# Kernel optimization log

Measured on AMD Instinct MI355X. Metric: run time of the kernel, lower is better.

The kernel has to match this reference:

```python
import jax, jax.numpy as jnp
import numpy as np

B, T, H, D = 1, 2048, 32, 128
Q_GROUP = 4
HKV = H // Q_GROUP
INNER = H * D
KV_INNER = HKV * D
ROPE_BASE = 10000.0
NEG = -1e30


def _rope_tables(seq_len, head_dim, dtype):
    inv_freq = 1.0 / (ROPE_BASE ** (jnp.arange(0, head_dim, 2, dtype=jnp.float32) / head_dim))
    t = jnp.arange(seq_len, dtype=jnp.float32)
    freqs = jnp.einsum('t,f->tf', t, inv_freq)          # [T, D/2]
    emb = jnp.concatenate([freqs, freqs], axis=-1)      # [T, D]
    cos = jnp.cos(emb)[None, :, None, :].astype(dtype)  # [1, T, 1, D]
    sin = jnp.sin(emb)[None, :, None, :].astype(dtype)
    return cos, sin


def _rotate(x, cos, sin):
    # x: [B, T, H, D]; split-half rotation: cat(-x2, x1)
    half = x.shape[-1] // 2
    x1, x2 = x[..., :half], x[..., half:]
    x_rot = jnp.concatenate([-x2, x1], axis=-1)
    return x * cos + x_rot * sin


def setup_inputs() -> dict:
    key = jax.random.key(0)
    ks = jax.random.split(key, 5)
    return {
        'stm': jax.random.normal(ks[0], (B, T, H, D), dtype=jnp.float32),
        'w_q': jax.random.normal(ks[1], (INNER, INNER), dtype=jnp.float32) * 0.02,
        'w_k': jax.random.normal(ks[2], (KV_INNER, INNER), dtype=jnp.float32) * 0.02,
        'w_v': jax.random.normal(ks[3], (KV_INNER, INNER), dtype=jnp.float32) * 0.02,
        'w_o': jax.random.normal(ks[4], (INNER, INNER), dtype=jnp.float32) * 0.02,
    }


def reference(stm, w_q, w_k, w_v, w_o):
    b, t, h, d = stm.shape
    x = stm.reshape(b * t, h * d)
    q = x @ w_q.T                                   # [B*T, H*D]
    k = x @ w_k.T                                   # [B*T, Hkv*D]
    v = x @ w_v.T
    # GQA repeat_interleave over query-group axis (broadcast then reshape)
    k = jnp.broadcast_to(k.reshape(b * t, HKV, 1, d), (b * t, HKV, Q_GROUP, d)).reshape(b, t, h, d)
    v = jnp.broadcast_to(v.reshape(b * t, HKV, 1, d), (b * t, HKV, Q_GROUP, d)).reshape(b, t, h, d)
    q = q.reshape(b, t, h, d)
    cos, sin = _rope_tables(t, d, stm.dtype)        # prefill: seq_start = 0
    q = _rotate(q, cos, sin)
    k = _rotate(k, cos, sin)                        # rotated k is what gets written to the KV cache
    scale = 1.0 / np.sqrt(d)
    scores = jnp.einsum('bqhd,bkhd->bhqk', q, k).astype(jnp.float32) * scale
    causal = jnp.tril(jnp.ones((t, t), dtype=jnp.float32))          # mask_w
    bias = (1.0 - causal) * NEG                                     # mask_b
    scores = scores * causal[None, None] + bias[None, None]
    attn = jax.nn.softmax(scores, axis=-1).astype(stm.dtype)
    o = jnp.einsum('bhqk,bkhd->bqhd', attn, v)
    o = o.reshape(b * t, h * d) @ w_o.T
    return o.reshape(b, t, h, d)
```

## Files before the change

kernel.cpp:

```cpp
#include <hip/hip_runtime.h>
#include <hip/hip_bf16.h>
#include <stdint.h>
#include <stddef.h>

using bf16  = __hip_bfloat16;
using v4s   = __attribute__((ext_vector_type(4))) short;
using v8s   = __attribute__((ext_vector_type(8))) short;
using f32x4 = __attribute__((ext_vector_type(4))) float;

#define MFMA_16x16x32(a, b, c) __builtin_amdgcn_mfma_f32_16x16x32_bf16((a), (b), (c), 0, 0, 0)

__device__ __forceinline__ void async_lds16(const bf16* g, bf16* l) {
  __builtin_amdgcn_global_load_lds(
      (const __attribute__((address_space(1))) void*)g,
      (__attribute__((address_space(3))) void*)l, 16, 0, 0);
}

__device__ __forceinline__ short bf16_bits(float f) {
  bf16 h = __float2bfloat16(f);
  short s;
  __builtin_memcpy(&s, &h, sizeof(s));
  return s;
}

__global__ void cvt_f32_bf16(const float* __restrict__ in, bf16* __restrict__ out,
                             int n4) {
  const int i = blockIdx.x * blockDim.x + threadIdx.x;
  if (i >= n4) return;
  const float4 f = ((const float4*)in)[i];
  v4s o;
  o[0] = bf16_bits(f.x);
  o[1] = bf16_bits(f.y);
  o[2] = bf16_bits(f.z);
  o[3] = bf16_bits(f.w);
  *(v4s*)(out + (size_t)i * 4) = o;
}

template <bool F32OUT>
__global__ __launch_bounds__(512, 2) void gemm_bt8(const bf16* __restrict__ A,
                                                   const bf16* __restrict__ B,
                                                   void* __restrict__ C,
                                                   int M, int N, int K) {
  __shared__ bf16 lds[2][64][512];
  const int tid  = threadIdx.x;
  const int w    = tid >> 6;
  const int lane = tid & 63;
  const int quad = lane >> 4;
  const int m16  = lane & 15;
  const int wr = w >> 2, wc = w & 3;
  const int tm = blockIdx.y, tn = blockIdx.x;
  const int NKT = K >> 6;

  const bf16* Ast0 = A + (size_t)(tm * 256 + w * 16 + m16) * K + quad * 8;
  const bf16* Ast1 = Ast0 + (size_t)128 * K;
  const bf16* Bst0 = B + (size_t)(tn * 256 + w * 16 + m16) * K + quad * 8;
  const bf16* Bst1 = Bst0 + (size_t)128 * K;

  auto stage = [&](const bf16* g, bf16* l) {
    async_lds16(g, l);
    async_lds16(g + 32, l + 512);
  };

  f32x4 acc[8][4] = {};

  {
    bf16* L0 = &lds[0][0][0];
    bf16* L1 = &lds[1][0][0];
    stage(Bst0, L0 + (32 + w * 2) * 512);
    stage(Bst1, L0 + (48 + w * 2) * 512);
    stage(Ast0, L0 + (w * 2) * 512);
    stage(Ast1, L0 + (16 + w * 2) * 512);
    stage(Bst0 + 64, L1 + (32 + w * 2) * 512);
    stage(Bst1 + 64, L1 + (48 + w * 2) * 512);
    stage(Ast0 + 64, L1 + (w * 2) * 512);
  }
  asm volatile("s_waitcnt vmcnt(6)" ::: "memory");
  __builtin_amdgcn_s_barrier();

  for (int k = 0; k < NKT; ++k) {
    bf16* Lc = &lds[k & 1][0][0];
    bf16* Ln = &lds[(k & 1) ^ 1][0][0];
    v8s af[4][2], bfv[4][2];
#pragma unroll
    for (int mi = 0; mi < 4; ++mi) {
      af[mi][0] = *(const v8s*)(Lc + ((wr * 8 + mi) * 2 + 0) * 512 + lane * 8);
      af[mi][1] = *(const v8s*)(Lc + ((wr * 8 + mi) * 2 + 1) * 512 + lane * 8);
    }
#pragma unroll
    for (int ni = 0; ni < 4; ++ni) {
      bfv[ni][0] = *(const v8s*)(Lc + (32 + (wc * 4 + ni) * 2 + 0) * 512 + lane * 8);
      bfv[ni][1] = *(const v8s*)(Lc + (32 + (wc * 4 + ni) * 2 + 1) * 512 + lane * 8);
    }
    if (k + 1 < NKT) stage(Ast1 + (size_t)(k + 1) * 64, Ln + (16 + w * 2) * 512);
    __builtin_amdgcn_s_barrier();
    asm volatile("s_waitcnt lgkmcnt(0)" ::: "memory");
    __builtin_amdgcn_sched_barrier(0);
    __builtin_amdgcn_s_setprio(1);
#pragma unroll
    for (int mi = 0; mi < 4; ++mi)
#pragma unroll
      for (int ni = 0; ni < 2; ++ni) {
        acc[mi][ni] = MFMA_16x16x32(af[mi][0], bfv[ni][0], acc[mi][ni]);
        acc[mi][ni] = MFMA_16x16x32(af[mi][1], bfv[ni][1], acc[mi][ni]);
      }
    __builtin_amdgcn_s_setprio(0);
    __builtin_amdgcn_s_barrier();
    if (k + 2 < NKT) stage(Bst0 + (size_t)(k + 2) * 64, Lc + (32 + w * 2) * 512);
    __builtin_amdgcn_s_barrier();
    __builtin_amdgcn_s_setprio(1);
#pragma unroll
    for (int mi = 0; mi < 4; ++mi)
#pragma unroll
      for (int ni = 2; ni < 4; ++ni) {
        acc[mi][ni] = MFMA_16x16x32(af[mi][0], bfv[ni][0], acc[mi][ni]);
        acc[mi][ni] = MFMA_16x16x32(af[mi][1], bfv[ni][1], acc[mi][ni]);
      }
    __builtin_amdgcn_s_setprio(0);
    __builtin_amdgcn_s_barrier();
#pragma unroll
    for (int mi = 0; mi < 4; ++mi) {
      af[mi][0] = *(const v8s*)(Lc + ((wr * 8 + 4 + mi) * 2 + 0) * 512 + lane * 8);
      af[mi][1] = *(const v8s*)(Lc + ((wr * 8 + 4 + mi) * 2 + 1) * 512 + lane * 8);
    }
    if (k + 2 < NKT) stage(Bst1 + (size_t)(k + 2) * 64, Lc + (48 + w * 2) * 512);
    __builtin_amdgcn_s_barrier();
    asm volatile("s_waitcnt lgkmcnt(0)" ::: "memory");
    __builtin_amdgcn_sched_barrier(0);
    __builtin_amdgcn_s_setprio(1);
#pragma unroll
    for (int mi = 0; mi < 4; ++mi)
#pragma unroll
      for (int ni = 0; ni < 2; ++ni) {
        acc[4 + mi][ni] = MFMA_16x16x32(af[mi][0], bfv[ni][0], acc[4 + mi][ni]);
        acc[4 + mi][ni] = MFMA_16x16x32(af[mi][1], bfv[ni][1], acc[4 + mi][ni]);
      }
    __builtin_amdgcn_s_setprio(0);
    __builtin_amdgcn_s_barrier();
    if (k + 2 < NKT) stage(Ast0 + (size_t)(k + 2) * 64, Lc + (w * 2) * 512);
    if (k < NKT - 2) {
      asm volatile("s_waitcnt vmcnt(6)" ::: "memory");
    } else {
      asm volatile("s_waitcnt vmcnt(0)" ::: "memory");
    }
    __builtin_amdgcn_s_barrier();
    __builtin_amdgcn_s_setprio(1);
#pragma unroll
    for (int mi = 0; mi < 4; ++mi)
#pragma unroll
      for (int ni = 2; ni < 4; ++ni) {
        acc[4 + mi][ni] = MFMA_16x16x32(af[mi][0], bfv[ni][0], acc[4 + mi][ni]);
        acc[4 + mi][ni] = MFMA_16x16x32(af[mi][1], bfv[ni][1], acc[4 + mi][ni]);
      }
    __builtin_amdgcn_s_setprio(0);
    __builtin_amdgcn_s_barrier();
  }

#pragma unroll
  for (int mi = 0; mi < 8; ++mi)
#pragma unroll
    for (int ni = 0; ni < 4; ++ni) {
      const int row = tm * 256 + wr * 128 + mi * 16 + quad * 4;
      const int col = tn * 256 + wc * 64 + ni * 16 + m16;
#pragma unroll
      for (int r = 0; r < 4; ++r) {
        if (F32OUT)
          ((float*)C)[(size_t)(row + r) * N + col] = acc[mi][ni][r];
        else
          ((bf16*)C)[(size_t)(row + r) * N + col] = __float2bfloat16(acc[mi][ni][r]);
      }
    }
}

__global__ void rope_kernel(bf16* __restrict__ qkv) {
  const int t  = blockIdx.x;
  const int hh = blockIdx.y;
  const int d  = threadIdx.x;
  const float invf = powf(10000.0f, -(float)(d & 63) * (1.0f / 64.0f));
  const float ang  = (float)t * invf;
  const float c = cosf(ang);
  const float s = sinf(ang);
  const bool isq = (hh < 32);
  bf16* ptr = qkv + (size_t)t * 6144 + (isq ? hh * 128 : 4096 + (hh - 32) * 128);
  const float x   = __bfloat162float(ptr[d]);
  const float xp  = __bfloat162float(ptr[d ^ 64]);
  __syncthreads();
  const float rot = (d < 64) ? -xp : xp;
  const float outv = (x * c + rot * s) * (isq ? 0.08838834764831845f : 1.0f);
  ptr[d] = __float2bfloat16(outv);
}

__global__ void vtrans_kernel(const bf16* __restrict__ qkv, bf16* __restrict__ vt) {
  __shared__ bf16 tile[32][34];
  const int t0 = blockIdx.x * 32, c0 = blockIdx.y * 32;
  const int tx = threadIdx.x, ty = threadIdx.y;
#pragma unroll
  for (int i = 0; i < 4; ++i)
    tile[ty + 8 * i][tx] = qkv[(size_t)(t0 + ty + 8 * i) * 6144 + 5120 + c0 + tx];
  __syncthreads();
#pragma unroll
  for (int i = 0; i < 4; ++i)
    vt[(size_t)(c0 + ty + 8 * i) * 2048 + t0 + tx] = tile[tx][ty + 8 * i];
}

__global__ __launch_bounds__(256) void attn_fused4(const bf16* __restrict__ QKV,
                                                   const bf16* __restrict__ Vt,
                                                   bf16* __restrict__ O) {
  const int bx = (int)blockIdx.x;
  const int h  = (int)blockIdx.y;
  const int qt = (h < 16) ? (15 - bx) : bx;
  const int hk = h >> 2;
  const int tid = threadIdx.x, w = tid >> 6, lane = tid & 63;
  const int quad = lane >> 4, m16 = lane & 15;
  __shared__ bf16 Ks[32 * 512];
  __shared__ bf16 Vs[32 * 512];
  __shared__ __attribute__((aligned(16))) short Ps[4][2048];
  short* Pw = Ps[w];

  v8s qf[2][4];
#pragma unroll
  for (int ni = 0; ni < 2; ++ni)
#pragma unroll
    for (int dk = 0; dk < 4; ++dk)
      qf[ni][dk] = *(const v8s*)(QKV + (size_t)(qt * 128 + w * 32 + ni * 16 + m16) * 6144 +
                                 h * 128 + dk * 32 + quad * 8);

  const bf16* kg = QKV + (size_t)m16 * 6144 + 4096 + hk * 128 + w * 32 + quad * 8;
  const bf16* vg = Vt + (size_t)(hk * 128 + m16) * 2048 + w * 32 + quad * 8;

  f32x4 acc[8][2] = {};
  float m_run[2] = {-1e30f, -1e30f}, l_run[2] = {0.f, 0.f};

#pragma unroll
  for (int mi = 0; mi < 8; ++mi)
    async_lds16(kg + (size_t)mi * 16 * 6144, &Ks[(mi * 4 + w) * 512]);
#pragma unroll
  for (int mi = 0; mi < 8; ++mi)
    async_lds16(vg + (size_t)mi * 16 * 2048, &Vs[(mi * 4 + w) * 512]);

  for (int kt = 0; kt <= qt; ++kt) {
    asm volatile("s_waitcnt vmcnt(8)" ::: "memory");
    __builtin_amdgcn_s_barrier();
    f32x4 s[8][2];
    __builtin_amdgcn_s_setprio(1);
#pragma unroll
    for (int mi = 0; mi < 8; ++mi) {
      s[mi][0] = f32x4{0.f, 0.f, 0.f, 0.f};
      s[mi][1] = f32x4{0.f, 0.f, 0.f, 0.f};
#pragma unroll
      for (int dk = 0; dk < 4; ++dk) {
        v8s af = *(const v8s*)&Ks[(mi * 4 + dk) * 512 + lane * 8];
        s[mi][0] = MFMA_16x16x32(af, qf[0][dk], s[mi][0]);
        s[mi][1] = MFMA_16x16x32(af, qf[1][dk], s[mi][1]);
      }
    }
    __builtin_amdgcn_s_setprio(0);
    asm volatile("s_waitcnt vmcnt(0)" ::: "memory");
    __builtin_amdgcn_s_barrier();
    if (kt < qt) {
      const bf16* kg2 = kg + (size_t)(kt + 1) * 128 * 6144;
#pragma unroll
      for (int mi = 0; mi < 8; ++mi)
        async_lds16(kg2 + (size_t)mi * 16 * 6144, &Ks[(mi * 4 + w) * 512]);
    }
    if (kt == qt) {
#pragma unroll
      for (int mi = 0; mi < 8; ++mi)
#pragma unroll
        for (int ni = 0; ni < 2; ++ni)
#pragma unroll
          for (int r = 0; r < 4; ++r)
            if (mi * 16 + quad * 4 + r > w * 32 + ni * 16 + m16) s[mi][ni][r] = -1e30f;
    }
#pragma unroll
    for (int ni = 0; ni < 2; ++ni) {
      float mx = -1e30f;
#pragma unroll
      for (int mi = 0; mi < 8; ++mi)
#pragma unroll
        for (int r = 0; r < 4; ++r) mx = fmaxf(mx, s[mi][ni][r]);
      mx = fmaxf(mx, __shfl_xor(mx, 16));
      mx = fmaxf(mx, __shfl_xor(mx, 32));
      const float mnew = fmaxf(m_run[ni], mx);
      const float alpha = __expf(m_run[ni] - mnew);
      m_run[ni] = mnew;
      float rs = 0.f;
#pragma unroll
      for (int mi = 0; mi < 8; ++mi)
#pragma unroll
        for (int r = 0; r < 4; ++r) {
          const float p = __expf(s[mi][ni][r] - mnew);
          s[mi][ni][r] = p;
          rs += p;
        }
      rs += __shfl_xor(rs, 16);
      rs += __shfl_xor(rs, 32);
      l_run[ni] = l_run[ni] * alpha + rs;
#pragma unroll
      for (int mi2 = 0; mi2 < 8; ++mi2)
#pragma unroll
        for (int r = 0; r < 4; ++r) acc[mi2][ni][r] *= alpha;
    }
#pragma unroll
    for (int mi = 0; mi < 4; ++mi)
#pragma unroll
      for (int ni = 0; ni < 2; ++ni) {
        v4s p4;
#pragma unroll
        for (int r = 0; r < 4; ++r) p4[r] = bf16_bits(s[mi][ni][r]);
        const int base = (ni * 2 + (mi >> 1)) * 512 +
                         ((mi & 1) * 2 + (quad >> 1)) * 128 + m16 * 8 + (quad & 1) * 4;
        *(v4s*)&Pw[base] = p4;
      }
    asm volatile("" ::: "memory");
    __builtin_amdgcn_s_setprio(1);
#pragma unroll
    for (int kpl = 0; kpl < 2; ++kpl) {
      v8s pf0 = *(const v8s*)&Pw[(0 * 2 + kpl) * 512 + lane * 8];
      v8s pf1 = *(const v8s*)&Pw[(1 * 2 + kpl) * 512 + lane * 8];
#pragma unroll
      for (int mi2 = 0; mi2 < 8; ++mi2) {
        v8s vf = *(const v8s*)&Vs[(mi2 * 4 + kpl) * 512 + lane * 8];
        acc[mi2][0] = MFMA_16x16x32(vf, pf0, acc[mi2][0]);
        acc[mi2][1] = MFMA_16x16x32(vf, pf1, acc[mi2][1]);
      }
    }
    __builtin_amdgcn_s_setprio(0);
    asm volatile("" ::: "memory");
#pragma unroll
    for (int mi = 4; mi < 8; ++mi)
#pragma unroll
      for (int ni = 0; ni < 2; ++ni) {
        const int mloc = mi - 4;
        v4s p4;
#pragma unroll
        for (int r = 0; r < 4; ++r) p4[r] = bf16_bits(s[mi][ni][r]);
        const int base = (ni * 2 + (mloc >> 1)) * 512 +
                         ((mloc & 1) * 2 + (quad >> 1)) * 128 + m16 * 8 + (quad & 1) * 4;
        *(v4s*)&Pw[base] = p4;
      }
    asm volatile("" ::: "memory");
    __builtin_amdgcn_s_setprio(1);
#pragma unroll
    for (int kpl = 0; kpl < 2; ++kpl) {
      v8s pf0 = *(const v8s*)&Pw[(0 * 2 + kpl) * 512 + lane * 8];
      v8s pf1 = *(const v8s*)&Pw[(1 * 2 + kpl) * 512 + lane * 8];
#pragma unroll
      for (int mi2 = 0; mi2 < 8; ++mi2) {
        v8s vf = *(const v8s*)&Vs[(mi2 * 4 + 2 + kpl) * 512 + lane * 8];
        acc[mi2][0] = MFMA_16x16x32(vf, pf0, acc[mi2][0]);
        acc[mi2][1] = MFMA_16x16x32(vf, pf1, acc[mi2][1]);
      }
    }
    __builtin_amdgcn_s_setprio(0);
    asm volatile("" ::: "memory");
    __builtin_amdgcn_s_barrier();
    if (kt < qt) {
      const bf16* vg2 = vg + (size_t)(kt + 1) * 128;
#pragma unroll
      for (int mi = 0; mi < 8; ++mi)
        async_lds16(vg2 + (size_t)mi * 16 * 2048, &Vs[(mi * 4 + w) * 512]);
    }
  }
#pragma unroll
  for (int ni = 0; ni < 2; ++ni) {
    const float rl = 1.0f / l_run[ni];
    const size_t qrow = qt * 128 + w * 32 + ni * 16 + m16;
#pragma unroll
    for (int mi2 = 0; mi2 < 8; ++mi2) {
      v4s o4;
#pragma unroll
      for (int r = 0; r < 4; ++r) o4[r] = bf16_bits(acc[mi2][ni][r] * rl);
      *(v4s*)(O + qrow * 4096 + h * 128 + mi2 * 16 + quad * 4) = o4;
    }
  }
}

extern "C" void kernel_launch(void* const* d_in, const int* in_sizes, int n_in,
                              void* d_out, int out_size, void* d_ws, size_t ws_size,
                              hipStream_t stream) {
  const float* stm = (const float*)d_in[0];
  const float* w_q = (const float*)d_in[1];
  const float* w_k = (const float*)d_in[2];
  const float* w_v = (const float*)d_in[3];
  const float* w_o = (const float*)d_in[4];
  float* out = (float*)d_out;

  const size_t M_STM = (size_t)2048 * 4096;
  const size_t M_WQ  = (size_t)4096 * 4096;
  const size_t M_WK  = (size_t)1024 * 4096;

  bf16* ws      = (bf16*)d_ws;
  bf16* wqkv_bf = ws;
  bf16* wo_bf   = ws;
  bf16* vT      = ws + M_WQ;
  bf16* stm_bf  = ws + 24 * 1024 * 1024;
  bf16* o_buf   = stm_bf;
  bf16* qkv_buf = ws + 32 * 1024 * 1024;

  cvt_f32_bf16<<<(int)(M_STM / 1024), 256, 0, stream>>>(stm, stm_bf, (int)(M_STM / 4));
  cvt_f32_bf16<<<(int)(M_WQ / 1024), 256, 0, stream>>>(w_q, wqkv_bf, (int)(M_WQ / 4));
  cvt_f32_bf16<<<(int)(M_WK / 1024), 256, 0, stream>>>(w_k, wqkv_bf + M_WQ, (int)(M_WK / 4));
  cvt_f32_bf16<<<(int)(M_WK / 1024), 256, 0, stream>>>(w_v, wqkv_bf + M_WQ + M_WK, (int)(M_WK / 4));

  gemm_bt8<false><<<dim3(24, 8), 512, 0, stream>>>(stm_bf, wqkv_bf, qkv_buf, 2048, 6144, 4096);

  cvt_f32_bf16<<<(int)(M_WQ / 1024), 256, 0, stream>>>(w_o, wo_bf, (int)(M_WQ / 4));

  rope_kernel<<<dim3(2048, 40), 128, 0, stream>>>(qkv_buf);
  vtrans_kernel<<<dim3(64, 32), dim3(32, 8), 0, stream>>>(qkv_buf, vT);
  attn_fused4<<<dim3(16, 32), 256, 0, stream>>>(qkv_buf, vT, o_buf);

  gemm_bt8<true><<<dim3(16, 8), 512, 0, stream>>>(o_buf, wo_bf, out, 2048, 4096, 4096);
}
```

Baseline: 627.8 us.

## Prefetch GEMM LDS fragments across phases and precompute RoPE cos/sin table

Restructures the 8-wave GEMM main loop so A/B fragment reads from LDS for the next k-tile are issued during the current tile's MFMA phases. The B fragments are split into two register sets and the MFMA phase order is reshuffled, which removes one barrier per phase and retunes the vmcnt waits. Separately, RoPE cos/sin values are computed once per (t, freq) into a table instead of with powf/sinf/cosf in every head's thread. This costs more registers in the GEMM and carries some risk of LDS read/write hazards across the reordered barriers.

```diff
diff --git a/kernel.cpp b/kernel.cpp
--- a/kernel.cpp
+++ b/kernel.cpp
@@ -37,7 +37,7 @@
 }
 
 template <bool F32OUT>
-__global__ __launch_bounds__(512, 2) void gemm_bt8(const bf16* __restrict__ A,
+__global__ __launch_bounds__(512, 2) void gemm_bt9(const bf16* __restrict__ A,
                                                    const bf16* __restrict__ B,
                                                    void* __restrict__ C,
                                                    int M, int N, int K) {
@@ -62,6 +62,9 @@
   };
 
   f32x4 acc[8][4] = {};
+  v8s af[4][2];
+  v8s bf01[2][2];
+  v8s bf23[2][2];
 
   {
     bf16* L0 = &lds[0][0][0];
@@ -76,23 +79,28 @@
   }
   asm volatile("s_waitcnt vmcnt(6)" ::: "memory");
   __builtin_amdgcn_s_barrier();
+  {
+    bf16* L0 = &lds[0][0][0];
+#pragma unroll
+    for (int mi = 0; mi < 4; ++mi)
+#pragma unroll
+      for (int kg = 0; kg < 2; ++kg)
+        af[mi][kg] = *(const v8s*)(L0 + ((wr * 8 + mi) * 2 + kg) * 512 + lane * 8);
+#pragma unroll
+    for (int ni = 0; ni < 2; ++ni)
+#pragma unroll
+      for (int kg = 0; kg < 2; ++kg) {
+        bf01[ni][kg] = *(const v8s*)(L0 + (32 + (wc * 4 + ni) * 2 + kg) * 512 + lane * 8);
+        bf23[ni][kg] = *(const v8s*)(L0 + (32 + (wc * 4 + 2 + ni) * 2 + kg) * 512 + lane * 8);
+      }
+  }
+  asm volatile("" ::: "memory");
 
   for (int k = 0; k < NKT; ++k) {
     bf16* Lc = &lds[k & 1][0][0];
     bf16* Ln = &lds[(k & 1) ^ 1][0][0];
-    v8s af[4][2], bfv[4][2];
-#pragma unroll
-    for (int mi = 0; mi < 4; ++mi) {
-      af[mi][0] = *(const v8s*)(Lc + ((wr * 8 + mi) * 2 + 0) * 512 + lane * 8);
-      af[mi][1] = *(const v8s*)(Lc + ((wr * 8 + mi) * 2 + 1) * 512 + lane * 8);
-    }
-#pragma unroll
-    for (int ni = 0; ni < 4; ++ni) {
-      bfv[ni][0] = *(const v8s*)(Lc + (32 + (wc * 4 + ni) * 2 + 0) * 512 + lane * 8);
-      bfv[ni][1] = *(const v8s*)(Lc + (32 + (wc * 4 + ni) * 2 + 1) * 512 + lane * 8);
-    }
+    __builtin_amdgcn_s_barrier();
     if (k + 1 < NKT) stage(Ast1 + (size_t)(k + 1) * 64, Ln + (16 + w * 2) * 512);
-    __builtin_amdgcn_s_barrier();
     asm volatile("s_waitcnt lgkmcnt(0)" ::: "memory");
     __builtin_amdgcn_sched_barrier(0);
     __builtin_amdgcn_s_setprio(1);
@@ -100,30 +108,36 @@
     for (int mi = 0; mi < 4; ++mi)
 #pragma unroll
       for (int ni = 0; ni < 2; ++ni) {
-        acc[mi][ni] = MFMA_16x16x32(af[mi][0], bfv[ni][0], acc[mi][ni]);
-        acc[mi][ni] = MFMA_16x16x32(af[mi][1], bfv[ni][1], acc[mi][ni]);
-      }
-    __builtin_amdgcn_s_setprio(0);
+        acc[mi][ni] = MFMA_16x16x32(af[mi][0], bf01[ni][0], acc[mi][ni]);
+        acc[mi][ni] = MFMA_16x16x32(af[mi][1], bf01[ni][1], acc[mi][ni]);
+      }
+    __builtin_amdgcn_s_setprio(0);
+    asm volatile("" ::: "memory");
     __builtin_amdgcn_s_barrier();
     if (k + 2 < NKT) stage(Bst0 + (size_t)(k + 2) * 64, Lc + (32 + w * 2) * 512);
-    __builtin_amdgcn_s_barrier();
-    __builtin_amdgcn_s_setprio(1);
-#pragma unroll
-    for (int mi = 0; mi < 4; ++mi)
-#pragma unroll
-      for (int ni = 2; ni < 4; ++ni) {
-        acc[mi][ni] = MFMA_16x16x32(af[mi][0], bfv[ni][0], acc[mi][ni]);
-        acc[mi][ni] = MFMA_16x16x32(af[mi][1], bfv[ni][1], acc[mi][ni]);
-      }
-    __builtin_amdgcn_s_setprio(0);
-    __builtin_amdgcn_s_barrier();
-#pragma unroll
-    for (int mi = 0; mi < 4; ++mi) {
-      af[mi][0] = *(const v8s*)(Lc + ((wr * 8 + 4 + mi) * 2 + 0) * 512 + lane * 8);
-      af[mi][1] = *(const v8s*)(Lc + ((wr * 8 + 4 + mi) * 2 + 1) * 512 + lane * 8);
-    }
+    __builtin_amdgcn_s_setprio(1);
+#pragma unroll
+    for (int mi = 0; mi < 4; ++mi)
+#pragma unroll
+      for (int ni = 0; ni < 2; ++ni) {
+        acc[mi][2 + ni] = MFMA_16x16x32(af[mi][0], bf23[ni][0], acc[mi][2 + ni]);
+        acc[mi][2 + ni] = MFMA_16x16x32(af[mi][1], bf23[ni][1], acc[mi][2 + ni]);
+      }
+    __builtin_amdgcn_s_setprio(0);
+    asm volatile("" ::: "memory");
+#pragma unroll
+    for (int mi = 0; mi < 4; ++mi)
+#pragma unroll
+      for (int kg = 0; kg < 2; ++kg)
+        af[mi][kg] = *(const v8s*)(Lc + ((wr * 8 + 4 + mi) * 2 + kg) * 512 + lane * 8);
+    asm volatile("" ::: "memory");
+    if (k + 2 < NKT) {
+      asm volatile("s_waitcnt vmcnt(6)" ::: "memory");
+    } else if (k + 1 < NKT) {
+      asm volatile("s_waitcnt vmcnt(4)" ::: "memory");
+    }
+    __builtin_amdgcn_s_barrier();
     if (k + 2 < NKT) stage(Bst1 + (size_t)(k + 2) * 64, Lc + (48 + w * 2) * 512);
-    __builtin_amdgcn_s_barrier();
     asm volatile("s_waitcnt lgkmcnt(0)" ::: "memory");
     __builtin_amdgcn_sched_barrier(0);
     __builtin_amdgcn_s_setprio(1);
@@ -131,28 +145,49 @@
     for (int mi = 0; mi < 4; ++mi)
 #pragma unroll
       for (int ni = 0; ni < 2; ++ni) {
-        acc[4 + mi][ni] = MFMA_16x16x32(af[mi][0], bfv[ni][0], acc[4 + mi][ni]);
-        acc[4 + mi][ni] = MFMA_16x16x32(af[mi][1], bfv[ni][1], acc[4 + mi][ni]);
-      }
-    __builtin_amdgcn_s_setprio(0);
+        acc[4 + mi][2 + ni] = MFMA_16x16x32(af[mi][0], bf23[ni][0], acc[4 + mi][2 + ni]);
+        acc[4 + mi][2 + ni] = MFMA_16x16x32(af[mi][1], bf23[ni][1], acc[4 + mi][2 + ni]);
+      }
+    __builtin_amdgcn_s_setprio(0);
+    asm volatile("" ::: "memory");
+    if (k + 1 < NKT) {
+#pragma unroll
+      for (int ni = 0; ni < 2; ++ni)
+#pragma unroll
+        for (int kg = 0; kg < 2; ++kg)
+          bf23[ni][kg] = *(const v8s*)(Ln + (32 + (wc * 4 + 2 + ni) * 2 + kg) * 512 + lane * 8);
+    }
+    asm volatile("" ::: "memory");
+    if (k + 2 < NKT) {
+      asm volatile("s_waitcnt vmcnt(4)" ::: "memory");
+    } else if (k + 1 < NKT) {
+      asm volatile("s_waitcnt vmcnt(0)" ::: "memory");
+    }
     __builtin_amdgcn_s_barrier();
     if (k + 2 < NKT) stage(Ast0 + (size_t)(k + 2) * 64, Lc + (w * 2) * 512);
-    if (k < NKT - 2) {
-      asm volatile("s_waitcnt vmcnt(6)" ::: "memory");
-    } else {
-      asm volatile("s_waitcnt vmcnt(0)" ::: "memory");
-    }
-    __builtin_amdgcn_s_barrier();
-    __builtin_amdgcn_s_setprio(1);
-#pragma unroll
-    for (int mi = 0; mi < 4; ++mi)
-#pragma unroll
-      for (int ni = 2; ni < 4; ++ni) {
-        acc[4 + mi][ni] = MFMA_16x16x32(af[mi][0], bfv[ni][0], acc[4 + mi][ni]);
-        acc[4 + mi][ni] = MFMA_16x16x32(af[mi][1], bfv[ni][1], acc[4 + mi][ni]);
-      }
-    __builtin_amdgcn_s_setprio(0);
-    __builtin_amdgcn_s_barrier();
+    __builtin_amdgcn_s_setprio(1);
+#pragma unroll
+    for (int mi = 0; mi < 4; ++mi)
+#pragma unroll
+      for (int ni = 0; ni < 2; ++ni) {
+        acc[4 + mi][ni] = MFMA_16x16x32(af[mi][0], bf01[ni][0], acc[4 + mi][ni]);
+        acc[4 + mi][ni] = MFMA_16x16x32(af[mi][1], bf01[ni][1], acc[4 + mi][ni]);
+      }
+    __builtin_amdgcn_s_setprio(0);
+    asm volatile("" ::: "memory");
+    if (k + 1 < NKT) {
+#pragma unroll
+      for (int mi = 0; mi < 4; ++mi)
+#pragma unroll
+        for (int kg = 0; kg < 2; ++kg)
+          af[mi][kg] = *(const v8s*)(Ln + ((wr * 8 + mi) * 2 + kg) * 512 + lane * 8);
+#pragma unroll
+      for (int ni = 0; ni < 2; ++ni)
+#pragma unroll
+        for (int kg = 0; kg < 2; ++kg)
+          bf01[ni][kg] = *(const v8s*)(Ln + (32 + (wc * 4 + ni) * 2 + kg) * 512 + lane * 8);
+    }
+    asm volatile("" ::: "memory");
   }
 
 #pragma unroll
@@ -171,14 +206,21 @@
     }
 }
 
-__global__ void rope_kernel(bf16* __restrict__ qkv) {
+__global__ void rope_tab(float2* __restrict__ tab) {
+  const int t = blockIdx.x;
+  const int f = threadIdx.x;
+  const float invf = powf(10000.0f, -(float)f * (1.0f / 64.0f));
+  const float ang  = (float)t * invf;
+  tab[t * 64 + f] = make_float2(cosf(ang), sinf(ang));
+}
+
+__global__ void rope_kernel(bf16* __restrict__ qkv, const float2* __restrict__ tab) {
   const int t  = blockIdx.x;
   const int hh = blockIdx.y;
   const int d  = threadIdx.x;
-  const float invf = powf(10000.0f, -(float)(d & 63) * (1.0f / 64.0f));
-  const float ang  = (float)t * invf;
-  const float c = cosf(ang);
-  const float s = sinf(ang);
+  const float2 cs = tab[t * 64 + (d & 63)];
+  const float c = cs.x;
+  const float s = cs.y;
   const bool isq = (hh < 32);
   bf16* ptr = qkv + (size_t)t * 6144 + (isq ? hh * 128 : 4096 + (hh - 32) * 128);
   const float x   = __bfloat162float(ptr[d]);
@@ -393,6 +435,7 @@
   bf16* wqkv_bf = ws;
   bf16* wo_bf   = ws;
   bf16* vT      = ws + M_WQ;
+  float2* ropeT = (float2*)(ws + 18 * 1024 * 1024);
   bf16* stm_bf  = ws + 24 * 1024 * 1024;
   bf16* o_buf   = stm_bf;
   bf16* qkv_buf = ws + 32 * 1024 * 1024;
@@ -402,13 +445,14 @@
   cvt_f32_bf16<<<(int)(M_WK / 1024), 256, 0, stream>>>(w_k, wqkv_bf + M_WQ, (int)(M_WK / 4));
   cvt_f32_bf16<<<(int)(M_WK / 1024), 256, 0, stream>>>(w_v, wqkv_bf + M_WQ + M_WK, (int)(M_WK / 4));
 
-  gemm_bt8<false><<<dim3(24, 8), 512, 0, stream>>>(stm_bf, wqkv_bf, qkv_buf, 2048, 6144, 4096);
+  gemm_bt9<false><<<dim3(24, 8), 512, 0, stream>>>(stm_bf, wqkv_bf, qkv_buf, 2048, 6144, 4096);
 
   cvt_f32_bf16<<<(int)(M_WQ / 1024), 256, 0, stream>>>(w_o, wo_bf, (int)(M_WQ / 4));
-
-  rope_kernel<<<dim3(2048, 40), 128, 0, stream>>>(qkv_buf);
+  rope_tab<<<2048, 64, 0, stream>>>(ropeT);
+
+  rope_kernel<<<dim3(2048, 40), 128, 0, stream>>>(qkv_buf, ropeT);
   vtrans_kernel<<<dim3(64, 32), dim3(32, 8), 0, stream>>>(qkv_buf, vT);
   attn_fused4<<<dim3(16, 32), 256, 0, stream>>>(qkv_buf, vT, o_buf);
 
-  gemm_bt8<true><<<dim3(16, 8), 512, 0, stream>>>(o_buf, wo_bf, out, 2048, 4096, 4096);
-}
+  gemm_bt9<true><<<dim3(16, 8), 512, 0, stream>>>(o_buf, wo_bf, out, 2048, 4096, 4096);
+}
```

After: 607.0 us. 3.3% less time.

## Simplify GEMM main loop to whole-tile double buffering and precompute RoPE table

Applied to the files above, without the earlier changes.

The GEMM loop used to stage and wait on partial A/B sub-tiles between four barrier-separated MFMA phases, with priority hints. It now stages whole K-tiles two ahead into the free LDS buffer, loads all fragments once and runs all 64 MFMAs per iteration with a single barrier pair. This cuts barrier and scheduling overhead, but loses finer-grained overlap of loads with compute. Separately, RoPE cos/sin values are computed once into a table by a small kernel instead of evaluating powf, sinf and cosf per element.

```diff
diff --git a/kernel.cpp b/kernel.cpp
--- a/kernel.cpp
+++ b/kernel.cpp
@@ -37,10 +37,10 @@
 }
 
 template <bool F32OUT>
-__global__ __launch_bounds__(512, 2) void gemm_bt8(const bf16* __restrict__ A,
-                                                   const bf16* __restrict__ B,
-                                                   void* __restrict__ C,
-                                                   int M, int N, int K) {
+__global__ __launch_bounds__(512, 2) void gemm_bt10(const bf16* __restrict__ A,
+                                                    const bf16* __restrict__ B,
+                                                    void* __restrict__ C,
+                                                    int M, int N, int K) {
   __shared__ bf16 lds[2][64][512];
   const int tid  = threadIdx.x;
   const int w    = tid >> 6;
@@ -60,98 +60,46 @@
     async_lds16(g, l);
     async_lds16(g + 32, l + 512);
   };
+  auto stage_tile = [&](int kt, bf16* L) {
+    stage(Ast0 + (size_t)kt * 64, L + (w * 2) * 512);
+    stage(Ast1 + (size_t)kt * 64, L + (16 + w * 2) * 512);
+    stage(Bst0 + (size_t)kt * 64, L + (32 + w * 2) * 512);
+    stage(Bst1 + (size_t)kt * 64, L + (48 + w * 2) * 512);
+  };
 
   f32x4 acc[8][4] = {};
 
-  {
-    bf16* L0 = &lds[0][0][0];
-    bf16* L1 = &lds[1][0][0];
-    stage(Bst0, L0 + (32 + w * 2) * 512);
-    stage(Bst1, L0 + (48 + w * 2) * 512);
-    stage(Ast0, L0 + (w * 2) * 512);
-    stage(Ast1, L0 + (16 + w * 2) * 512);
-    stage(Bst0 + 64, L1 + (32 + w * 2) * 512);
-    stage(Bst1 + 64, L1 + (48 + w * 2) * 512);
-    stage(Ast0 + 64, L1 + (w * 2) * 512);
-  }
-  asm volatile("s_waitcnt vmcnt(6)" ::: "memory");
+  stage_tile(0, &lds[0][0][0]);
+  if (NKT > 1) stage_tile(1, &lds[1][0][0]);
+  asm volatile("s_waitcnt vmcnt(8)" ::: "memory");
   __builtin_amdgcn_s_barrier();
 
   for (int k = 0; k < NKT; ++k) {
     bf16* Lc = &lds[k & 1][0][0];
-    bf16* Ln = &lds[(k & 1) ^ 1][0][0];
-    v8s af[4][2], bfv[4][2];
-#pragma unroll
-    for (int mi = 0; mi < 4; ++mi) {
-      af[mi][0] = *(const v8s*)(Lc + ((wr * 8 + mi) * 2 + 0) * 512 + lane * 8);
-      af[mi][1] = *(const v8s*)(Lc + ((wr * 8 + mi) * 2 + 1) * 512 + lane * 8);
-    }
-#pragma unroll
-    for (int ni = 0; ni < 4; ++ni) {
-      bfv[ni][0] = *(const v8s*)(Lc + (32 + (wc * 4 + ni) * 2 + 0) * 512 + lane * 8);
-      bfv[ni][1] = *(const v8s*)(Lc + (32 + (wc * 4 + ni) * 2 + 1) * 512 + lane * 8);
-    }
-    if (k + 1 < NKT) stage(Ast1 + (size_t)(k + 1) * 64, Ln + (16 + w * 2) * 512);
-    __builtin_amdgcn_s_barrier();
+    v8s bfr[4][2];
+#pragma unroll
+    for (int ni = 0; ni < 4; ++ni)
+#pragma unroll
+      for (int kg = 0; kg < 2; ++kg)
+        bfr[ni][kg] = *(const v8s*)(Lc + (32 + (wc * 4 + ni) * 2 + kg) * 512 + lane * 8);
+#pragma unroll
+    for (int mi = 0; mi < 8; ++mi) {
+      v8s a0 = *(const v8s*)(Lc + ((wr * 8 + mi) * 2 + 0) * 512 + lane * 8);
+      v8s a1 = *(const v8s*)(Lc + ((wr * 8 + mi) * 2 + 1) * 512 + lane * 8);
+#pragma unroll
+      for (int ni = 0; ni < 4; ++ni) {
+        acc[mi][ni] = MFMA_16x16x32(a0, bfr[ni][0], acc[mi][ni]);
+        acc[mi][ni] = MFMA_16x16x32(a1, bfr[ni][1], acc[mi][ni]);
+      }
+    }
     asm volatile("s_waitcnt lgkmcnt(0)" ::: "memory");
-    __builtin_amdgcn_sched_barrier(0);
-    __builtin_amdgcn_s_setprio(1);
-#pragma unroll
-    for (int mi = 0; mi < 4; ++mi)
-#pragma unroll
-      for (int ni = 0; ni < 2; ++ni) {
-        acc[mi][ni] = MFMA_16x16x32(af[mi][0], bfv[ni][0], acc[mi][ni]);
-        acc[mi][ni] = MFMA_16x16x32(af[mi][1], bfv[ni][1], acc[mi][ni]);
-      }
-    __builtin_amdgcn_s_setprio(0);
-    __builtin_amdgcn_s_barrier();
-    if (k + 2 < NKT) stage(Bst0 + (size_t)(k + 2) * 64, Lc + (32 + w * 2) * 512);
-    __builtin_amdgcn_s_barrier();
-    __builtin_amdgcn_s_setprio(1);
-#pragma unroll
-    for (int mi = 0; mi < 4; ++mi)
-#pragma unroll
-      for (int ni = 2; ni < 4; ++ni) {
-        acc[mi][ni] = MFMA_16x16x32(af[mi][0], bfv[ni][0], acc[mi][ni]);
-        acc[mi][ni] = MFMA_16x16x32(af[mi][1], bfv[ni][1], acc[mi][ni]);
-      }
-    __builtin_amdgcn_s_setprio(0);
-    __builtin_amdgcn_s_barrier();
-#pragma unroll
-    for (int mi = 0; mi < 4; ++mi) {
-      af[mi][0] = *(const v8s*)(Lc + ((wr * 8 + 4 + mi) * 2 + 0) * 512 + lane * 8);
-      af[mi][1] = *(const v8s*)(Lc + ((wr * 8 + 4 + mi) * 2 + 1) * 512 + lane * 8);
-    }
-    if (k + 2 < NKT) stage(Bst1 + (size_t)(k + 2) * 64, Lc + (48 + w * 2) * 512);
-    __builtin_amdgcn_s_barrier();
-    asm volatile("s_waitcnt lgkmcnt(0)" ::: "memory");
-    __builtin_amdgcn_sched_barrier(0);
-    __builtin_amdgcn_s_setprio(1);
-#pragma unroll
-    for (int mi = 0; mi < 4; ++mi)
-#pragma unroll
-      for (int ni = 0; ni < 2; ++ni) {
-        acc[4 + mi][ni] = MFMA_16x16x32(af[mi][0], bfv[ni][0], acc[4 + mi][ni]);
-        acc[4 + mi][ni] = MFMA_16x16x32(af[mi][1], bfv[ni][1], acc[4 + mi][ni]);
-      }
-    __builtin_amdgcn_s_setprio(0);
-    __builtin_amdgcn_s_barrier();
-    if (k + 2 < NKT) stage(Ast0 + (size_t)(k + 2) * 64, Lc + (w * 2) * 512);
-    if (k < NKT - 2) {
-      asm volatile("s_waitcnt vmcnt(6)" ::: "memory");
-    } else {
+    __builtin_amdgcn_s_barrier();
+    if (k + 2 < NKT) stage_tile(k + 2, Lc);
+    if (k + 2 < NKT) {
+      asm volatile("s_waitcnt vmcnt(8)" ::: "memory");
+    } else if (k + 1 < NKT) {
       asm volatile("s_waitcnt vmcnt(0)" ::: "memory");
     }
-    __builtin_amdgcn_s_barrier();
-    __builtin_amdgcn_s_setprio(1);
-#pragma unroll
-    for (int mi = 0; mi < 4; ++mi)
-#pragma unroll
-      for (int ni = 2; ni < 4; ++ni) {
-        acc[4 + mi][ni] = MFMA_16x16x32(af[mi][0], bfv[ni][0], acc[4 + mi][ni]);
-        acc[4 + mi][ni] = MFMA_16x16x32(af[mi][1], bfv[ni][1], acc[4 + mi][ni]);
-      }
-    __builtin_amdgcn_s_setprio(0);
     __builtin_amdgcn_s_barrier();
   }
 
@@ -171,14 +119,21 @@
     }
 }
 
-__global__ void rope_kernel(bf16* __restrict__ qkv) {
+__global__ void rope_tab(float2* __restrict__ tab) {
+  const int t = blockIdx.x;
+  const int f = threadIdx.x;
+  const float invf = powf(10000.0f, -(float)f * (1.0f / 64.0f));
+  const float ang  = (float)t * invf;
+  tab[t * 64 + f] = make_float2(cosf(ang), sinf(ang));
+}
+
+__global__ void rope_kernel(bf16* __restrict__ qkv, const float2* __restrict__ tab) {
   const int t  = blockIdx.x;
   const int hh = blockIdx.y;
   const int d  = threadIdx.x;
-  const float invf = powf(10000.0f, -(float)(d & 63) * (1.0f / 64.0f));
-  const float ang  = (float)t * invf;
-  const float c = cosf(ang);
-  const float s = sinf(ang);
+  const float2 cs = tab[t * 64 + (d & 63)];
+  const float c = cs.x;
+  const float s = cs.y;
   const bool isq = (hh < 32);
   bf16* ptr = qkv + (size_t)t * 6144 + (isq ? hh * 128 : 4096 + (hh - 32) * 128);
   const float x   = __bfloat162float(ptr[d]);
@@ -393,6 +348,7 @@
   bf16* wqkv_bf = ws;
   bf16* wo_bf   = ws;
   bf16* vT      = ws + M_WQ;
+  float2* ropeT = (float2*)(ws + 18 * 1024 * 1024);
   bf16* stm_bf  = ws + 24 * 1024 * 1024;
   bf16* o_buf   = stm_bf;
   bf16* qkv_buf = ws + 32 * 1024 * 1024;
@@ -402,13 +358,14 @@
   cvt_f32_bf16<<<(int)(M_WK / 1024), 256, 0, stream>>>(w_k, wqkv_bf + M_WQ, (int)(M_WK / 4));
   cvt_f32_bf16<<<(int)(M_WK / 1024), 256, 0, stream>>>(w_v, wqkv_bf + M_WQ + M_WK, (int)(M_WK / 4));
 
-  gemm_bt8<false><<<dim3(24, 8), 512, 0, stream>>>(stm_bf, wqkv_bf, qkv_buf, 2048, 6144, 4096);
+  gemm_bt10<false><<<dim3(24, 8), 512, 0, stream>>>(stm_bf, wqkv_bf, qkv_buf, 2048, 6144, 4096);
 
   cvt_f32_bf16<<<(int)(M_WQ / 1024), 256, 0, stream>>>(w_o, wo_bf, (int)(M_WQ / 4));
-
-  rope_kernel<<<dim3(2048, 40), 128, 0, stream>>>(qkv_buf);
+  rope_tab<<<2048, 64, 0, stream>>>(ropeT);
+
+  rope_kernel<<<dim3(2048, 40), 128, 0, stream>>>(qkv_buf, ropeT);
   vtrans_kernel<<<dim3(64, 32), dim3(32, 8), 0, stream>>>(qkv_buf, vT);
   attn_fused4<<<dim3(16, 32), 256, 0, stream>>>(qkv_buf, vT, o_buf);
 
-  gemm_bt8<true><<<dim3(16, 8), 512, 0, stream>>>(o_buf, wo_bf, out, 2048, 4096, 4096);
-}
+  gemm_bt10<true><<<dim3(16, 8), 512, 0, stream>>>(o_buf, wo_bf, out, 2048, 4096, 4096);
+}
```

Measured after the change: 660.6 us. 1.05x slower.
